# Kernel tuning notes

Measured on AMD Instinct MI355X. Metric: run time of the kernel, lower is better.

Reference implementation:

```python
import jax, jax.numpy as jnp
import numpy as np

HIDDEN = 2048
NH = 32        # query heads
NKV = 4        # kv heads
D = 128        # head dim
T = 2048       # tokens
WINDOW = 512   # sliding window
EPS = 1e-6
THETA = 1000000.0
SCALE = D ** -0.5


def setup_inputs() -> dict:
    key = jax.random.key(0)
    k1, k2, k3 = jax.random.split(key, 3)
    return {
        "positions": jnp.arange(T, dtype=jnp.int64) if jax.config.jax_enable_x64 else jnp.arange(T, dtype=jnp.int32),
        "hidden_states": jax.random.normal(k1, (T, HIDDEN), dtype=jnp.float32),
        "w_qkv": jax.random.normal(k2, (HIDDEN, (NH + 2 * NKV) * D), dtype=jnp.float32) * 0.02,
        "w_o": jax.random.normal(k3, (NH * D, HIDDEN), dtype=jnp.float32) * 0.02,
        "q_norm_w": jnp.ones((D,), dtype=jnp.float32),
        "k_norm_w": jnp.ones((D,), dtype=jnp.float32),
    }


def _rms_norm(x, w):
    # x: [..., D]; per-head RMSNorm
    var = jnp.mean(x * x, axis=-1, keepdims=True)
    return x * jax.lax.rsqrt(var + EPS) * w


def _rope(x, positions):
    # x: [T, H, D], neox-style rotary over full head dim
    inv_freq = 1.0 / (THETA ** (jnp.arange(0, D, 2, dtype=jnp.float32) / D))  # [D/2]
    freqs = positions.astype(jnp.float32)[:, None] * inv_freq                 # [T, D/2]
    cos = jnp.cos(freqs)[:, None, :]
    sin = jnp.sin(freqs)[:, None, :]
    x1, x2 = x[..., : D // 2], x[..., D // 2 :]
    return jnp.concatenate([x1 * cos - x2 * sin, x2 * cos + x1 * sin], axis=-1)


def reference(positions, hidden_states, w_qkv, w_o, q_norm_w, k_norm_w):
    qkv = hidden_states @ w_qkv                                   # [T, (NH+2NKV)*D]
    q, k, v = jnp.split(qkv, [NH * D, (NH + NKV) * D], axis=-1)
    q = _rms_norm(q.reshape(T, NH, D), q_norm_w)
    k = _rms_norm(k.reshape(T, NKV, D), k_norm_w)
    v = v.reshape(T, NKV, D)
    q = _rope(q, positions)
    k = _rope(k, positions)
    # GQA: expand kv heads to query heads
    rep = NH // NKV
    k = jnp.repeat(k, rep, axis=1)                                # [T, NH, D]
    v = jnp.repeat(v, rep, axis=1)
    scores = jnp.einsum("qhd,khd->hqk", q, k) * SCALE             # [NH, T, T]
    i = jnp.arange(T)[:, None]
    j = jnp.arange(T)[None, :]
    mask = (j <= i) & (i - j < WINDOW)                            # causal sliding window
    scores = jnp.where(mask[None, :, :], scores, jnp.finfo(scores.dtype).min)
    probs = jax.nn.softmax(scores, axis=-1)
    out = jnp.einsum("hqk,khd->qhd", probs, v).reshape(T, NH * D)
    return out @ w_o
```

## Files before the change

### kernel.cpp

```cpp
#include <hip/hip_runtime.h>
#include <math.h>

#define T      2048
#define HIDDEN 2048
#define NH     32
#define NKV    4
#define D      128
#define WINDOW 512
#define QKVW   ((NH + 2 * NKV) * D)
#define ODIM   (NH * D)
#define EPS    1e-6f
#define SCALE  0.08838834764831845f
#define PSTR   68
#define ESTR   136
#define VSTR   36
#define QMUL   ((float)(0.08838834764831845 * 1.4426950408889634))
#define MLOG2E 5.7707801635558536f

typedef _Float16 f16x8 __attribute__((ext_vector_type(8)));
typedef _Float16 f16x4 __attribute__((ext_vector_type(4)));
typedef float    f32x4 __attribute__((ext_vector_type(4)));


__device__ __forceinline__ void gl2lds16(const void* g, void* l) {
  __builtin_amdgcn_global_load_lds((const __attribute__((address_space(1))) void*)g,
                                   (__attribute__((address_space(3))) void*)l,
                                   16, 0, 0);
}

#define NB_A  2048
#define NB_B1 5120
#define NB_B2 4096
__global__ __launch_bounds__(256)
void prep(const float* __restrict__ hidden, const float* __restrict__ w_qkv,
          const float* __restrict__ w_o, const int* __restrict__ positions,
          _Float16* __restrict__ Ah1, _Float16* __restrict__ Bp1,
          _Float16* __restrict__ Bp2, float* __restrict__ cosT,
          float* __restrict__ sinT) {
  const int bx = blockIdx.x;
  const int tid = threadIdx.x;
  if (bx < NB_A) {
    const int cid = bx * 256 + tid;
    const int c = cid & 63;
    const int tile = cid >> 6;
    const int mtg = tile & (T / 16 - 1);
    const int kt = tile >> 7;
    const float* src = hidden + (size_t)(mtg * 16 + (c & 15)) * HIDDEN + kt * 32 + (c >> 4) * 8;
    const float4 a = *(const float4*)src;
    const float4 b = *(const float4*)(src + 4);
    f16x8 h;
    h[0] = (_Float16)a.x; h[1] = (_Float16)a.y; h[2] = (_Float16)a.z; h[3] = (_Float16)a.w;
    h[4] = (_Float16)b.x; h[5] = (_Float16)b.y; h[6] = (_Float16)b.z; h[7] = (_Float16)b.w;
    *(f16x8*)(Ah1 + (size_t)cid * 8) = h;
  } else if (bx < NB_A + NB_B1) {
    const int cid = (bx - NB_A) * 256 + tid;
    const int c = cid & 63;
    const int tile = cid >> 6;
    const int ntg = tile % (QKVW >> 4);
    const int kt = tile / (QKVW >> 4);
    const float* src = w_qkv + (size_t)(kt * 32 + (c >> 4) * 8) * QKVW + ntg * 16 + (c & 15);
    f16x8 h;
#pragma unroll
    for (int j = 0; j < 8; ++j) h[j] = (_Float16)src[(size_t)j * QKVW];
    *(f16x8*)(Bp1 + (size_t)cid * 8) = h;
  } else if (bx < NB_A + NB_B1 + NB_B2) {
    const int cid = (bx - NB_A - NB_B1) * 256 + tid;
    const int c = cid & 63;
    const int tile = cid >> 6;
    const int ntg = tile & (HIDDEN / 16 - 1);
    const int kt = tile >> 7;
    const float* src = w_o + (size_t)(kt * 32 + (c >> 4) * 8) * HIDDEN + ntg * 16 + (c & 15);
    f16x8 h;
#pragma unroll
    for (int j = 0; j < 8; ++j) h[j] = (_Float16)src[(size_t)j * HIDDEN];
    *(f16x8*)(Bp2 + (size_t)cid * 8) = h;
  } else {
    const int p0 = (bx - NB_A - NB_B1 - NB_B2) * 64 + (tid >> 6) * 16;
    const int j = tid & 63;
    const float invf = (float)pow(1.0e6, -(double)j / 64.0);
#pragma unroll 4
    for (int i = 0; i < 16; ++i) {
      const int t = p0 + i;
      const float ang = (float)positions[t] * invf;
      cosT[t * 64 + j] = cosf(ang);
      sinT[t * 64 + j] = sinf(ang);
    }
  }
}

__global__ __launch_bounds__(256)
void gemm_qkv(const _Float16* __restrict__ Apk, const _Float16* __restrict__ Bpk,
              const float* __restrict__ qnw, const float* __restrict__ knw,
              const float* __restrict__ cosT, const float* __restrict__ sinT,
              _Float16* __restrict__ Qpk, _Float16* __restrict__ Kpk,
              _Float16* __restrict__ Vpk) {
  constexpr int NKT = HIDDEN / 32;
  __shared__ _Float16 SM[18432];
  _Float16* As = SM;
  _Float16* Bs = SM + 8192;

  const int tid = threadIdx.x;
  const int lane = tid & 63;
  const int wv = tid >> 6;
  const int l15 = lane & 15;
  const int l4 = lane >> 4;
  const int bx = blockIdx.x, by = blockIdx.y;

  f32x4 acc[2][8];
#pragma unroll
  for (int i = 0; i < 2; ++i)
#pragma unroll
    for (int j = 0; j < 8; ++j) acc[i][j] = (f32x4)0.f;

  const size_t Astep = (size_t)(T >> 4) * 1024;
  const size_t Bstep = (size_t)(QKVW >> 4) * 1024;
  const char* Ag = (const char*)Apk + (size_t)(by * 8) * 1024 + lane * 16;
  const char* Bg = (const char*)Bpk + (size_t)(bx * 8) * 1024 + lane * 16;

  for (int kt2 = 0; kt2 < NKT; kt2 += 2) {
    const char* a0 = Ag + (size_t)kt2 * Astep;
    const char* b0 = Bg + (size_t)kt2 * Bstep;
#pragma unroll
    for (int t = wv; t < 32; t += 4) {
      const int half = t >= 16;
      const int tt = half ? t - 16 : t;
      if (tt < 8)
        gl2lds16(a0 + half * Astep + (size_t)tt * 1024,
                 (char*)As + (half * 8 + tt) * 1024);
      else
        gl2lds16(b0 + half * Bstep + (size_t)(tt - 8) * 1024,
                 (char*)Bs + (half * 8 + (tt - 8)) * 1024);
    }
    __syncthreads();
#pragma unroll
    for (int h2 = 0; h2 < 2; ++h2) {
      f16x8 af[2], bf[8];
#pragma unroll
      for (int i = 0; i < 2; ++i)
        af[i] = *(const f16x8*)(As + (h2 * 8 + wv * 2 + i) * 512 + lane * 8);
#pragma unroll
      for (int j = 0; j < 8; ++j)
        bf[j] = *(const f16x8*)(Bs + (h2 * 8 + j) * 512 + lane * 8);
#pragma unroll
      for (int i = 0; i < 2; ++i)
#pragma unroll
        for (int j = 0; j < 8; ++j)
          acc[i][j] = __builtin_amdgcn_mfma_f32_16x16x32_f16(af[i], bf[j], acc[i][j], 0, 0, 0);
    }
    __syncthreads();
  }

  if (bx < NH + NKV) {
    const bool isq = bx < NH;
    const float* w = isq ? qnw : knw;
    const float omul = isq ? QMUL : 1.0f;
    float wcol[8];
#pragma unroll
    for (int j = 0; j < 8; ++j) wcol[j] = w[j * 16 + l15];

    _Float16* ex = SM + wv * (32 * ESTR);
#pragma unroll
    for (int i = 0; i < 2; ++i)
#pragma unroll
      for (int r = 0; r < 4; ++r) {
        float ss = 0.f;
#pragma unroll
        for (int j = 0; j < 8; ++j) ss += acc[i][j][r] * acc[i][j][r];
        ss += __shfl_xor(ss, 1); ss += __shfl_xor(ss, 2);
        ss += __shfl_xor(ss, 4); ss += __shfl_xor(ss, 8);
        const float rn = 1.0f / sqrtf(ss * (1.0f / D) + EPS);
        const int row = i * 16 + l4 * 4 + r;
        const int t = by * 128 + wv * 32 + row;
#pragma unroll
        for (int j = 0; j < 4; ++j) {
          const int jc = j * 16 + l15;
          const float c = cosT[t * 64 + jc];
          const float s = sinT[t * 64 + jc];
          const float x1 = acc[i][j][r] * rn * wcol[j];
          const float x2 = acc[i][j + 4][r] * rn * wcol[j + 4];
          ex[row * ESTR + jc]      = (_Float16)((x1 * c - x2 * s) * omul);
          ex[row * ESTR + 64 + jc] = (_Float16)((x2 * c + x1 * s) * omul);
        }
      }
    const int hl = isq ? bx : bx - NH;
    _Float16* dst0 = isq ? Qpk : Kpk;
#pragma unroll
    for (int u = 0; u < 2; ++u) {
      const int qt = by * 8 + wv * 2 + u;
#pragma unroll
      for (int ds = 0; ds < 4; ++ds) {
        const f16x8 frag = *(const f16x8*)(ex + (u * 16 + l15) * ESTR + ds * 32 + l4 * 8);
        *(f16x8*)(dst0 + ((size_t)(hl * 128 + qt) * 4 + ds) * 512 + lane * 8) = frag;
      }
    }
  } else {
    const int kvh = bx - NH - NKV;
    _Float16* exv = SM + wv * (128 * VSTR);
#pragma unroll
    for (int i = 0; i < 2; ++i)
#pragma unroll
      for (int j = 0; j < 8; ++j) {
        f16x4 v4;
#pragma unroll
        for (int r = 0; r < 4; ++r) v4[r] = (_Float16)acc[i][j][r];
        *(f16x4*)(exv + (j * 16 + l15) * VSTR + i * 16 + l4 * 4) = v4;
      }
    const int kt64 = by * 2 + (wv >> 1);
    const int ks = wv & 1;
#pragma unroll
    for (int dt = 0; dt < 8; ++dt) {
      const f16x4 lo = *(const f16x4*)(exv + (dt * 16 + l15) * VSTR + l4 * 8);
      const f16x4 hi = *(const f16x4*)(exv + (dt * 16 + l15) * VSTR + l4 * 8 + 4);
      f16x8 h8;
#pragma unroll
      for (int r = 0; r < 4; ++r) { h8[r] = lo[r]; h8[r + 4] = hi[r]; }
      *(f16x8*)(Vpk + (((size_t)(kvh * 32 + kt64) * 2 + ks) * 8 + dt) * 512 + lane * 8) = h8;
    }
  }
}

template<int BN>
__global__ __launch_bounds__(256)
void gemm_f16(const _Float16* __restrict__ Apk, const _Float16* __restrict__ Bpk,
              float* __restrict__ C0, float* __restrict__ C1,
              int M, int N, int nkt) {
  constexpr int BM = 128;
  constexpr int AT = BM / 16;
  constexpr int BT = BN / 16;
  constexpr int RT = 4;
  constexpr int CT = BN / 32;
  __shared__ _Float16 As[2 * AT * 512];
  __shared__ _Float16 Bs[2 * BT * 512];

  const int tid = threadIdx.x;
  const int lane = tid & 63;
  const int wv = tid >> 6;
  const int wr = wv & 1, wc = wv >> 1;
  const int kt0 = blockIdx.z * nkt;
  float* __restrict__ C = blockIdx.z ? C1 : C0;

  f32x4 acc[RT][CT];
#pragma unroll
  for (int i = 0; i < RT; ++i)
#pragma unroll
    for (int j = 0; j < CT; ++j) acc[i][j] = (f32x4)0.f;

  const size_t Astep = (size_t)(M >> 4) * 1024;
  const size_t Bstep = (size_t)(N >> 4) * 1024;
  const char* Ag = (const char*)Apk + (size_t)kt0 * Astep +
                   (size_t)(blockIdx.y * AT) * 1024 + lane * 16;
  const char* Bg = (const char*)Bpk + (size_t)kt0 * Bstep +
                   (size_t)(blockIdx.x * BT) * 1024 + lane * 16;

  for (int kt2 = 0; kt2 < nkt; kt2 += 2) {
    const char* a0 = Ag + (size_t)kt2 * Astep;
    const char* b0 = Bg + (size_t)kt2 * Bstep;
#pragma unroll
    for (int t = wv; t < 2 * (AT + BT); t += 4) {
      const int half = t >= (AT + BT);
      const int tt = half ? t - (AT + BT) : t;
      if (tt < AT)
        gl2lds16(a0 + half * Astep + (size_t)tt * 1024,
                 (char*)As + (half * AT + tt) * 1024);
      else
        gl2lds16(b0 + half * Bstep + (size_t)(tt - AT) * 1024,
                 (char*)Bs + (half * BT + (tt - AT)) * 1024);
    }
    __syncthreads();

#pragma unroll
    for (int h2 = 0; h2 < 2; ++h2) {
      f16x8 af[RT], bf[CT];
#pragma unroll
      for (int i = 0; i < RT; ++i)
        af[i] = *(const f16x8*)((const char*)As + (h2 * AT + wr * RT + i) * 1024 + lane * 16);
#pragma unroll
      for (int j = 0; j < CT; ++j)
        bf[j] = *(const f16x8*)((const char*)Bs + (h2 * BT + wc * CT + j) * 1024 + lane * 16);
#pragma unroll
      for (int i = 0; i < RT; ++i)
#pragma unroll
        for (int j = 0; j < CT; ++j)
          acc[i][j] = __builtin_amdgcn_mfma_f32_16x16x32_f16(af[i], bf[j], acc[i][j], 0, 0, 0);
    }
    __syncthreads();
  }

  const int row0 = blockIdx.y * BM + wr * 64 + ((lane >> 4) << 2);
  const int col0 = blockIdx.x * BN + wc * (CT * 16) + (lane & 15);
#pragma unroll
  for (int i = 0; i < RT; ++i)
#pragma unroll
    for (int j = 0; j < CT; ++j) {
#pragma unroll
      for (int r = 0; r < 4; ++r)
        C[(size_t)(row0 + i * 16 + r) * N + col0 + j * 16] = acc[i][j][r];
    }
}

__global__ __launch_bounds__(256)
void reduce_add(const float4* __restrict__ a, const float4* __restrict__ b,
                float4* __restrict__ o, int n4) {
  for (int i = blockIdx.x * 256 + threadIdx.x; i < n4; i += gridDim.x * 256) {
    const float4 x = a[i], y = b[i];
    o[i] = make_float4(x.x + y.x, x.y + y.y, x.z + y.z, x.w + y.w);
  }
}

__global__ __launch_bounds__(256)
void attn_mfma(const _Float16* __restrict__ Qpk, const _Float16* __restrict__ Kpk,
               const _Float16* __restrict__ Vpk, _Float16* __restrict__ Ap2) {
  const int h = blockIdx.x;
  const int q0 = blockIdx.y * 128;
  const int kvh = h >> 3;
  const int tid = threadIdx.x;
  const int lane = tid & 63;
  const int wv = tid >> 6;
  const int l15 = lane & 15;
  const int l4 = lane >> 4;

  __shared__ _Float16 SM[8192 + 8192 + 4 * 32 * PSTR];
  _Float16* Ks = SM;
  _Float16* Vs = SM + 8192;
  _Float16* Pw = SM + 16384 + wv * 32 * PSTR;

  f16x8 qfA[4], qfB[4];
  {
    const _Float16* qa = Qpk + ((size_t)h * 128 + (q0 >> 4) + wv * 2) * 2048 + lane * 8;
#pragma unroll
    for (int ds = 0; ds < 4; ++ds) {
      qfA[ds] = *(const f16x8*)(qa + ds * 512);
      qfB[ds] = *(const f16x8*)(qa + 2048 + ds * 512);
    }
  }

  f16x8 ones;
#pragma unroll
  for (int j = 0; j < 8; ++j) ones[j] = (_Float16)1.0f;

  f32x4 OA[8], OB[8];
#pragma unroll
  for (int dt = 0; dt < 8; ++dt) { OA[dt] = (f32x4)0.f; OB[dt] = (f32x4)0.f; }
  f32x4 LA = (f32x4)0.f, LB = (f32x4)0.f;

  int kstart = q0 - (WINDOW - 1);
  if (kstart < 0) kstart = 0;
  kstart &= ~63;

  for (int kt = kstart; kt < q0 + 128; kt += 64) {
    __syncthreads();
    const _Float16* Kg = Kpk + ((size_t)kvh * 128 + (kt >> 4)) * 2048 + lane * 8;
    const _Float16* Vg = Vpk + ((size_t)kvh * 32 + (kt >> 6)) * 8192 + lane * 8;
#pragma unroll
    for (int t = wv; t < 16; t += 4) {
      gl2lds16(Kg + t * 512, (char*)Ks + t * 1024);
      gl2lds16(Vg + t * 512, (char*)Vs + t * 1024);
    }
    __syncthreads();

    f32x4 sA[4], sB[4];
#pragma unroll
    for (int nt = 0; nt < 4; ++nt) { sA[nt] = (f32x4)(-MLOG2E); sB[nt] = (f32x4)(-MLOG2E); }
#pragma unroll
    for (int ds = 0; ds < 4; ++ds) {
#pragma unroll
      for (int nt = 0; nt < 4; ++nt) {
        const f16x8 kf = *(const f16x8*)(Ks + (nt * 4 + ds) * 512 + lane * 8);
        sA[nt] = __builtin_amdgcn_mfma_f32_16x16x32_f16(qfA[ds], kf, sA[nt], 0, 0, 0);
        sB[nt] = __builtin_amdgcn_mfma_f32_16x16x32_f16(qfB[ds], kf, sB[nt], 0, 0, 0);
      }
    }

    const int qbA = q0 + wv * 32 + l4 * 4;
    const int kb = kt + l15;
#pragma unroll
    for (int nt = 0; nt < 4; ++nt) {
      const int kidx = kb + nt * 16;
#pragma unroll
      for (int r = 0; r < 4; ++r) {
        float pA = __builtin_amdgcn_exp2f(sA[nt][r]);
        float pB = __builtin_amdgcn_exp2f(sB[nt][r]);
        pA = ((unsigned)(qbA + r - kidx) < WINDOW) ? pA : 0.f;
        pB = ((unsigned)(qbA + 16 + r - kidx) < WINDOW) ? pB : 0.f;
        Pw[(l4 * 4 + r) * PSTR + nt * 16 + l15] = (_Float16)pA;
        Pw[(16 + l4 * 4 + r) * PSTR + nt * 16 + l15] = (_Float16)pB;
      }
    }

#pragma unroll
    for (int ks = 0; ks < 2; ++ks) {
      const f16x8 pfA = *(const f16x8*)(Pw + l15 * PSTR + ks * 32 + l4 * 8);
      const f16x8 pfB = *(const f16x8*)(Pw + (16 + l15) * PSTR + ks * 32 + l4 * 8);
      LA = __builtin_amdgcn_mfma_f32_16x16x32_f16(pfA, ones, LA, 0, 0, 0);
      LB = __builtin_amdgcn_mfma_f32_16x16x32_f16(pfB, ones, LB, 0, 0, 0);
#pragma unroll
      for (int dt = 0; dt < 8; ++dt) {
        const f16x8 vf = *(const f16x8*)(Vs + (ks * 8 + dt) * 512 + lane * 8);
        OA[dt] = __builtin_amdgcn_mfma_f32_16x16x32_f16(pfA, vf, OA[dt], 0, 0, 0);
        OB[dt] = __builtin_amdgcn_mfma_f32_16x16x32_f16(pfB, vf, OB[dt], 0, 0, 0);
      }
    }
  }

  __syncthreads();
  _Float16* Tw = SM + wv * 16 * ESTR;
#pragma unroll
  for (int half = 0; half < 2; ++half) {
    const f32x4* O = half ? OB : OA;
    const f32x4  L = half ? LB : LA;
    float inv[4];
#pragma unroll
    for (int r = 0; r < 4; ++r) inv[r] = 1.0f / L[r];
#pragma unroll
    for (int dt = 0; dt < 8; ++dt)
#pragma unroll
      for (int r = 0; r < 4; ++r)
        Tw[(l4 * 4 + r) * ESTR + dt * 16 + l15] = (_Float16)(O[dt][r] * inv[r]);
    const int qt = (q0 >> 4) + wv * 2 + half;
#pragma unroll
    for (int ds = 0; ds < 4; ++ds) {
      const f16x8 frag = *(const f16x8*)(Tw + l15 * ESTR + ds * 32 + l4 * 8);
      *(f16x8*)(Ap2 + ((size_t)(h * 4 + ds) * 128 + qt) * 512 + lane * 8) = frag;
    }
  }
}

extern "C" void kernel_launch(void* const* d_in, const int* in_sizes, int n_in,
                              void* d_out, int out_size, void* d_ws, size_t ws_size,
                              hipStream_t stream) {
  const int*   positions = (const int*)d_in[0];
  const float* hidden    = (const float*)d_in[1];
  const float* w_qkv     = (const float*)d_in[2];
  const float* w_o       = (const float*)d_in[3];
  const float* q_norm_w  = (const float*)d_in[4];
  const float* k_norm_w  = (const float*)d_in[5];
  float* out = (float*)d_out;

  char* ws = (char*)d_ws;
  _Float16* Kpk = (_Float16*)ws;
  _Float16* Vpk = Kpk + (size_t)T * NKV * D;
  ws += (size_t)T * QKVW * 4;
  _Float16* Ap2 = (_Float16*)ws;
  float* P0 = (float*)(ws + (size_t)T * ODIM * 2);
  ws += (size_t)T * ODIM * 4;
  float* cosT = (float*)ws;  ws += (size_t)T * 64 * 4;
  float* sinT = (float*)ws;  ws += (size_t)T * 64 * 4;
  _Float16* Bp1 = (_Float16*)ws; ws += (size_t)HIDDEN * QKVW * 2;
  _Float16* Bp2 = (_Float16*)ws; ws += (size_t)ODIM * HIDDEN * 2;
  _Float16* Ah1 = (_Float16*)ws; ws += (size_t)T * HIDDEN * 2;
  _Float16* Qpk = (_Float16*)ws;
  float* P1 = (float*)Qpk;
  ws += (size_t)T * ODIM * 2;

  prep<<<dim3(NB_A + NB_B1 + NB_B2 + T / 64), 256, 0, stream>>>(
      hidden, w_qkv, w_o, positions, Ah1, Bp1, Bp2, cosT, sinT);

  gemm_qkv<<<dim3(QKVW / 128, T / 128), 256, 0, stream>>>(
      Ah1, Bp1, q_norm_w, k_norm_w, cosT, sinT, Qpk, Kpk, Vpk);

  attn_mfma<<<dim3(NH, T / 128), 256, 0, stream>>>(Qpk, Kpk, Vpk, Ap2);

  gemm_f16<128><<<dim3(HIDDEN / 128, T / 128, 2), 256, 0, stream>>>(
      Ap2, Bp2, P0, P1, T, HIDDEN, ODIM / 32 / 2);
  reduce_add<<<dim3(512), 256, 0, stream>>>((const float4*)P0, (const float4*)P1,
                                            (float4*)out, T * HIDDEN / 4);
}
```

Measured before the change: 300.0 us.

## Rewrite QKV GEMM as 256x256 tile with 4-stage async LDS pipeline

```diff
diff --git a/kernel.cpp b/kernel.cpp
--- a/kernel.cpp
+++ b/kernel.cpp
@@ -13,7 +13,6 @@
 #define SCALE  0.08838834764831845f
 #define PSTR   68
 #define ESTR   136
-#define VSTR   36
 #define QMUL   ((float)(0.08838834764831845 * 1.4426950408889634))
 #define MLOG2E 5.7707801635558536f
 
@@ -88,79 +87,105 @@
   }
 }
 
-__global__ __launch_bounds__(256)
+#define KSTEPS 64
+
+__global__ __launch_bounds__(512, 2)
 void gemm_qkv(const _Float16* __restrict__ Apk, const _Float16* __restrict__ Bpk,
               const float* __restrict__ qnw, const float* __restrict__ knw,
               const float* __restrict__ cosT, const float* __restrict__ sinT,
               _Float16* __restrict__ Qpk, _Float16* __restrict__ Kpk,
               _Float16* __restrict__ Vpk) {
-  constexpr int NKT = HIDDEN / 32;
-  __shared__ _Float16 SM[18432];
-  _Float16* As = SM;
-  _Float16* Bs = SM + 8192;
-
+  extern __shared__ _Float16 SM[];
   const int tid = threadIdx.x;
   const int lane = tid & 63;
   const int wv = tid >> 6;
+  const int wr = wv & 3;
+  const int wc = wv >> 2;
   const int l15 = lane & 15;
   const int l4 = lane >> 4;
   const int bx = blockIdx.x, by = blockIdx.y;
 
-  f32x4 acc[2][8];
-#pragma unroll
-  for (int i = 0; i < 2; ++i)
+  f32x4 acc[4][8];
+#pragma unroll
+  for (int i = 0; i < 4; ++i)
 #pragma unroll
     for (int j = 0; j < 8; ++j) acc[i][j] = (f32x4)0.f;
 
-  const size_t Astep = (size_t)(T >> 4) * 1024;
-  const size_t Bstep = (size_t)(QKVW >> 4) * 1024;
-  const char* Ag = (const char*)Apk + (size_t)(by * 8) * 1024 + lane * 16;
-  const char* Bg = (const char*)Bpk + (size_t)(bx * 8) * 1024 + lane * 16;
-
-  for (int kt2 = 0; kt2 < NKT; kt2 += 2) {
-    const char* a0 = Ag + (size_t)kt2 * Astep;
-    const char* b0 = Bg + (size_t)kt2 * Bstep;
-#pragma unroll
-    for (int t = wv; t < 32; t += 4) {
-      const int half = t >= 16;
-      const int tt = half ? t - 16 : t;
-      if (tt < 8)
-        gl2lds16(a0 + half * Astep + (size_t)tt * 1024,
-                 (char*)As + (half * 8 + tt) * 1024);
-      else
-        gl2lds16(b0 + half * Bstep + (size_t)(tt - 8) * 1024,
-                 (char*)Bs + (half * 8 + (tt - 8)) * 1024);
-    }
-    __syncthreads();
-#pragma unroll
-    for (int h2 = 0; h2 < 2; ++h2) {
-      f16x8 af[2], bf[8];
-#pragma unroll
-      for (int i = 0; i < 2; ++i)
-        af[i] = *(const f16x8*)(As + (h2 * 8 + wv * 2 + i) * 512 + lane * 8);
-#pragma unroll
-      for (int j = 0; j < 8; ++j)
-        bf[j] = *(const f16x8*)(Bs + (h2 * 8 + j) * 512 + lane * 8);
-#pragma unroll
-      for (int i = 0; i < 2; ++i)
-#pragma unroll
-        for (int j = 0; j < 8; ++j)
-          acc[i][j] = __builtin_amdgcn_mfma_f32_16x16x32_f16(af[i], bf[j], acc[i][j], 0, 0, 0);
-    }
-    __syncthreads();
-  }
-
-  if (bx < NH + NKV) {
-    const bool isq = bx < NH;
+  const int u0 = wv * 4;
+
+  auto stage = [&](int k, int s) {
+    const int u = u0 + s;
+    char* dst = (char*)SM + (k & 3) * 32768 +
+                (u < 16 ? u * 1024 : 16384 + (u - 16) * 1024);
+    const char* src = (u < 16)
+        ? (const char*)Apk + ((size_t)k * (T / 16) + by * 16 + u) * 1024 + lane * 16
+        : (const char*)Bpk + ((size_t)k * (QKVW / 16) + bx * 16 + (u - 16)) * 1024 + lane * 16;
+    gl2lds16(src, dst);
+  };
+
+#pragma unroll
+  for (int k = 0; k < 3; ++k)
+#pragma unroll
+    for (int s = 0; s < 4; ++s) stage(k, s);
+  asm volatile("s_waitcnt vmcnt(8)" ::: "memory");
+  __builtin_amdgcn_s_barrier();
+  __builtin_amdgcn_sched_barrier(0);
+
+  for (int t = 0; t < KSTEPS; ++t) {
+    const _Float16* As = SM + (t & 3) * 16384;
+    const _Float16* Bs = As + 8192;
+    f16x8 af[4], bf[8];
+#pragma unroll
+    for (int i = 0; i < 4; ++i)
+      af[i] = *(const f16x8*)(As + (wr * 4 + i) * 512 + lane * 8);
+#pragma unroll
+    for (int j = 0; j < 4; ++j)
+      bf[j] = *(const f16x8*)(Bs + (wc * 8 + j) * 512 + lane * 8);
+    if (t + 3 < KSTEPS) { stage(t + 3, 0); stage(t + 3, 1); }
+    __builtin_amdgcn_s_barrier();
+    __builtin_amdgcn_sched_barrier(0);
+    __builtin_amdgcn_s_setprio(1);
+#pragma unroll
+    for (int i = 0; i < 4; ++i)
+#pragma unroll
+      for (int j = 0; j < 4; ++j)
+        acc[i][j] = __builtin_amdgcn_mfma_f32_16x16x32_f16(af[i], bf[j], acc[i][j], 0, 0, 0);
+    __builtin_amdgcn_s_setprio(0);
+    __builtin_amdgcn_s_barrier();
+    __builtin_amdgcn_sched_barrier(0);
+#pragma unroll
+    for (int j = 4; j < 8; ++j)
+      bf[j] = *(const f16x8*)(Bs + (wc * 8 + j) * 512 + lane * 8);
+    if (t + 3 < KSTEPS) { stage(t + 3, 2); stage(t + 3, 3); }
+    __builtin_amdgcn_s_barrier();
+    __builtin_amdgcn_sched_barrier(0);
+    __builtin_amdgcn_s_setprio(1);
+#pragma unroll
+    for (int i = 0; i < 4; ++i)
+#pragma unroll
+      for (int j = 4; j < 8; ++j)
+        acc[i][j] = __builtin_amdgcn_mfma_f32_16x16x32_f16(af[i], bf[j], acc[i][j], 0, 0, 0);
+    __builtin_amdgcn_s_setprio(0);
+    if (t < KSTEPS - 3)       asm volatile("s_waitcnt vmcnt(8)" ::: "memory");
+    else if (t == KSTEPS - 3) asm volatile("s_waitcnt vmcnt(4)" ::: "memory");
+    else if (t == KSTEPS - 2) asm volatile("s_waitcnt vmcnt(0)" ::: "memory");
+    __builtin_amdgcn_s_barrier();
+    __builtin_amdgcn_sched_barrier(0);
+  }
+  __syncthreads();
+
+  const int hb = bx * 2 + wc;
+  if (hb < NH + NKV) {
+    const bool isq = hb < NH;
     const float* w = isq ? qnw : knw;
     const float omul = isq ? QMUL : 1.0f;
     float wcol[8];
 #pragma unroll
     for (int j = 0; j < 8; ++j) wcol[j] = w[j * 16 + l15];
 
-    _Float16* ex = SM + wv * (32 * ESTR);
-#pragma unroll
-    for (int i = 0; i < 2; ++i)
+    _Float16* ex = SM + wv * 8704;
+#pragma unroll
+    for (int i = 0; i < 4; ++i)
 #pragma unroll
       for (int r = 0; r < 4; ++r) {
         float ss = 0.f;
@@ -170,23 +195,23 @@
         ss += __shfl_xor(ss, 4); ss += __shfl_xor(ss, 8);
         const float rn = 1.0f / sqrtf(ss * (1.0f / D) + EPS);
         const int row = i * 16 + l4 * 4 + r;
-        const int t = by * 128 + wv * 32 + row;
+        const int tok = by * 256 + wr * 64 + row;
 #pragma unroll
         for (int j = 0; j < 4; ++j) {
           const int jc = j * 16 + l15;
-          const float c = cosT[t * 64 + jc];
-          const float s = sinT[t * 64 + jc];
+          const float c = cosT[tok * 64 + jc];
+          const float s = sinT[tok * 64 + jc];
           const float x1 = acc[i][j][r] * rn * wcol[j];
           const float x2 = acc[i][j + 4][r] * rn * wcol[j + 4];
           ex[row * ESTR + jc]      = (_Float16)((x1 * c - x2 * s) * omul);
           ex[row * ESTR + 64 + jc] = (_Float16)((x2 * c + x1 * s) * omul);
         }
       }
-    const int hl = isq ? bx : bx - NH;
+    const int hl = isq ? hb : hb - NH;
     _Float16* dst0 = isq ? Qpk : Kpk;
 #pragma unroll
-    for (int u = 0; u < 2; ++u) {
-      const int qt = by * 8 + wv * 2 + u;
+    for (int u = 0; u < 4; ++u) {
+      const int qt = by * 16 + wr * 4 + u;
 #pragma unroll
       for (int ds = 0; ds < 4; ++ds) {
         const f16x8 frag = *(const f16x8*)(ex + (u * 16 + l15) * ESTR + ds * 32 + l4 * 8);
@@ -194,28 +219,29 @@
       }
     }
   } else {
-    const int kvh = bx - NH - NKV;
-    _Float16* exv = SM + wv * (128 * VSTR);
-#pragma unroll
-    for (int i = 0; i < 2; ++i)
+    const int kvh = hb - NH - NKV;
+    _Float16* exv = SM + wv * 8704;
+#pragma unroll
+    for (int i = 0; i < 4; ++i)
 #pragma unroll
       for (int j = 0; j < 8; ++j) {
         f16x4 v4;
 #pragma unroll
         for (int r = 0; r < 4; ++r) v4[r] = (_Float16)acc[i][j][r];
-        *(f16x4*)(exv + (j * 16 + l15) * VSTR + i * 16 + l4 * 4) = v4;
-      }
-    const int kt64 = by * 2 + (wv >> 1);
-    const int ks = wv & 1;
-#pragma unroll
-    for (int dt = 0; dt < 8; ++dt) {
-      const f16x4 lo = *(const f16x4*)(exv + (dt * 16 + l15) * VSTR + l4 * 8);
-      const f16x4 hi = *(const f16x4*)(exv + (dt * 16 + l15) * VSTR + l4 * 8 + 4);
-      f16x8 h8;
-#pragma unroll
-      for (int r = 0; r < 4; ++r) { h8[r] = lo[r]; h8[r + 4] = hi[r]; }
-      *(f16x8*)(Vpk + (((size_t)(kvh * 32 + kt64) * 2 + ks) * 8 + dt) * 512 + lane * 8) = h8;
-    }
+        *(f16x4*)(exv + (j * 16 + l15) * 68 + i * 16 + l4 * 4) = v4;
+      }
+    const int kt64 = by * 4 + wr;
+#pragma unroll
+    for (int ks = 0; ks < 2; ++ks)
+#pragma unroll
+      for (int dt = 0; dt < 8; ++dt) {
+        const f16x4 lo = *(const f16x4*)(exv + (dt * 16 + l15) * 68 + ks * 32 + l4 * 8);
+        const f16x4 hi = *(const f16x4*)(exv + (dt * 16 + l15) * 68 + ks * 32 + l4 * 8 + 4);
+        f16x8 h8;
+#pragma unroll
+        for (int r = 0; r < 4; ++r) { h8[r] = lo[r]; h8[r + 4] = hi[r]; }
+        *(f16x8*)(Vpk + (((size_t)(kvh * 32 + kt64) * 2 + ks) * 8 + dt) * 512 + lane * 8) = h8;
+      }
   }
 }
 
@@ -455,7 +481,7 @@
   prep<<<dim3(NB_A + NB_B1 + NB_B2 + T / 64), 256, 0, stream>>>(
       hidden, w_qkv, w_o, positions, Ah1, Bp1, Bp2, cosT, sinT);
 
-  gemm_qkv<<<dim3(QKVW / 128, T / 128), 256, 0, stream>>>(
+  gemm_qkv<<<dim3(QKVW / 256, T / 256), 512, 139264, stream>>>(
       Ah1, Bp1, q_norm_w, k_norm_w, cosT, sinT, Qpk, Kpk, Vpk);
 
   attn_mfma<<<dim3(NH, T / 128), 256, 0, stream>>>(Qpk, Kpk, Vpk, Ap2);
```

Result: no change. 295.9 us (-1.3%).

## Triple-buffer QKV GEMM LDS loads with async prefetch and one barrier per step

Applied to the files above, without the earlier changes.

```diff
diff --git a/kernel.cpp b/kernel.cpp
--- a/kernel.cpp
+++ b/kernel.cpp
@@ -88,17 +88,15 @@
   }
 }
 
-__global__ __launch_bounds__(256)
+#define KSTEPS 64
+
+__global__ __launch_bounds__(256, 3)
 void gemm_qkv(const _Float16* __restrict__ Apk, const _Float16* __restrict__ Bpk,
               const float* __restrict__ qnw, const float* __restrict__ knw,
               const float* __restrict__ cosT, const float* __restrict__ sinT,
               _Float16* __restrict__ Qpk, _Float16* __restrict__ Kpk,
               _Float16* __restrict__ Vpk) {
-  constexpr int NKT = HIDDEN / 32;
-  __shared__ _Float16 SM[18432];
-  _Float16* As = SM;
-  _Float16* Bs = SM + 8192;
-
+  extern __shared__ _Float16 SM[];
   const int tid = threadIdx.x;
   const int lane = tid & 63;
   const int wv = tid >> 6;
@@ -112,43 +110,52 @@
 #pragma unroll
     for (int j = 0; j < 8; ++j) acc[i][j] = (f32x4)0.f;
 
-  const size_t Astep = (size_t)(T >> 4) * 1024;
-  const size_t Bstep = (size_t)(QKVW >> 4) * 1024;
-  const char* Ag = (const char*)Apk + (size_t)(by * 8) * 1024 + lane * 16;
-  const char* Bg = (const char*)Bpk + (size_t)(bx * 8) * 1024 + lane * 16;
-
-  for (int kt2 = 0; kt2 < NKT; kt2 += 2) {
-    const char* a0 = Ag + (size_t)kt2 * Astep;
-    const char* b0 = Bg + (size_t)kt2 * Bstep;
-#pragma unroll
-    for (int t = wv; t < 32; t += 4) {
-      const int half = t >= 16;
-      const int tt = half ? t - 16 : t;
-      if (tt < 8)
-        gl2lds16(a0 + half * Astep + (size_t)tt * 1024,
-                 (char*)As + (half * 8 + tt) * 1024);
-      else
-        gl2lds16(b0 + half * Bstep + (size_t)(tt - 8) * 1024,
-                 (char*)Bs + (half * 8 + (tt - 8)) * 1024);
-    }
-    __syncthreads();
-#pragma unroll
-    for (int h2 = 0; h2 < 2; ++h2) {
-      f16x8 af[2], bf[8];
-#pragma unroll
-      for (int i = 0; i < 2; ++i)
-        af[i] = *(const f16x8*)(As + (h2 * 8 + wv * 2 + i) * 512 + lane * 8);
+  auto stage = [&](int k, int s) {
+    const int u = wv * 4 + s;
+    char* dst = (char*)SM + (k % 3) * 16384 +
+                (u < 8 ? u * 1024 : 8192 + (u - 8) * 1024);
+    const char* src = (u < 8)
+        ? (const char*)Apk + ((size_t)k * (T / 16) + by * 8 + u) * 1024 + lane * 16
+        : (const char*)Bpk + ((size_t)k * (QKVW / 16) + bx * 8 + (u - 8)) * 1024 + lane * 16;
+    gl2lds16(src, dst);
+  };
+
+#pragma unroll
+  for (int k = 0; k < 2; ++k)
+#pragma unroll
+    for (int s = 0; s < 4; ++s) stage(k, s);
+  asm volatile("s_waitcnt vmcnt(4)" ::: "memory");
+  __builtin_amdgcn_s_barrier();
+  __builtin_amdgcn_sched_barrier(0);
+
+  int slot = 0;
+  for (int t = 0; t < KSTEPS; ++t) {
+    const _Float16* As = SM + slot * 8192;
+    const _Float16* Bs = As + 4096;
+    f16x8 af[2], bf[8];
+#pragma unroll
+    for (int i = 0; i < 2; ++i)
+      af[i] = *(const f16x8*)(As + (wv * 2 + i) * 512 + lane * 8);
+#pragma unroll
+    for (int j = 0; j < 8; ++j)
+      bf[j] = *(const f16x8*)(Bs + j * 512 + lane * 8);
+    if (t + 2 < KSTEPS)
+#pragma unroll
+      for (int s = 0; s < 4; ++s) stage(t + 2, s);
+    __builtin_amdgcn_s_setprio(1);
+#pragma unroll
+    for (int i = 0; i < 2; ++i)
 #pragma unroll
       for (int j = 0; j < 8; ++j)
-        bf[j] = *(const f16x8*)(Bs + (h2 * 8 + j) * 512 + lane * 8);
-#pragma unroll
-      for (int i = 0; i < 2; ++i)
-#pragma unroll
-        for (int j = 0; j < 8; ++j)
-          acc[i][j] = __builtin_amdgcn_mfma_f32_16x16x32_f16(af[i], bf[j], acc[i][j], 0, 0, 0);
-    }
-    __syncthreads();
-  }
+        acc[i][j] = __builtin_amdgcn_mfma_f32_16x16x32_f16(af[i], bf[j], acc[i][j], 0, 0, 0);
+    __builtin_amdgcn_s_setprio(0);
+    if (t < KSTEPS - 2)       asm volatile("s_waitcnt vmcnt(4)" ::: "memory");
+    else if (t == KSTEPS - 2) asm volatile("s_waitcnt vmcnt(0)" ::: "memory");
+    __builtin_amdgcn_s_barrier();
+    __builtin_amdgcn_sched_barrier(0);
+    slot = (slot == 2) ? 0 : slot + 1;
+  }
+  __syncthreads();
 
   if (bx < NH + NKV) {
     const bool isq = bx < NH;
@@ -455,7 +462,7 @@
   prep<<<dim3(NB_A + NB_B1 + NB_B2 + T / 64), 256, 0, stream>>>(
       hidden, w_qkv, w_o, positions, Ah1, Bp1, Bp2, cosT, sinT);
 
-  gemm_qkv<<<dim3(QKVW / 128, T / 128), 256, 0, stream>>>(
+  gemm_qkv<<<dim3(QKVW / 128, T / 128), 256, 49152, stream>>>(
       Ah1, Bp1, q_norm_w, k_norm_w, cosT, sinT, Qpk, Kpk, Vpk);
 
   attn_mfma<<<dim3(NH, T / 128), 256, 0, stream>>>(Qpk, Kpk, Vpk, Ap2);
```

Measured after the change: 290.3 us. -3.2%, faster.
